# Kernel optimization log

Measured on AMD Instinct MI355X. Metric: run time of the kernel, lower is better.

## Reference

```python
import jax, jax.numpy as jnp
import numpy as np

DIM = 64
H = 4
POS_DIM = 4
NUM_IDS = 16
B = 2048
N = 64


def setup_inputs() -> dict:
    key = jax.random.key(0)
    ks = jax.random.split(key, 16)
    d8 = DIM // 8
    stdv = 1.0 / np.sqrt(DIM * DIM)
    inp = {
        "x": jax.random.normal(ks[0], (B, N, DIM), jnp.float32),
        "pos": jax.random.normal(ks[1], (B, N, POS_DIM), jnp.float32),
        "strength": jax.random.normal(ks[2], (512,), jnp.float32),
        "embed_id1": 3,
        # weights stored [in, out] (torch Linear weight transposed)
        "Wq": jax.random.normal(ks[3], (DIM, DIM), jnp.float32) * 0.05,
        "Wk": jax.random.normal(ks[4], (DIM, DIM), jnp.float32) * 0.05,
        "pos_W1": jax.random.normal(ks[5], (POS_DIM, POS_DIM), jnp.float32) * 0.3,
        "pos_b1": jnp.zeros((POS_DIM,), jnp.float32),
        "pos_W2": jax.random.normal(ks[6], (POS_DIM, d8), jnp.float32) * 0.3,
        "pos_b2": jnp.zeros((d8,), jnp.float32),
        "head_W": jax.random.normal(ks[7], (d8, H), jnp.float32) * 0.3,
        "head_b": jnp.zeros((H,), jnp.float32),
        "gate": jnp.ones((H,), jnp.float32),
        "embeds": jax.random.uniform(ks[8], (NUM_IDS, DIM * DIM), jnp.float32, -stdv, stdv),
        "out_W": jax.random.normal(ks[9], (DIM, DIM), jnp.float32) * 0.05,
        "out_b": jnp.zeros((DIM,), jnp.float32),
        "str_W": jax.random.normal(ks[10], (512, 64), jnp.float32) * 0.04,
        "str_b": jnp.zeros((64,), jnp.float32),
    }
    return inp


def reference(x, pos, strength, embed_id1, Wq, Wk, pos_W1, pos_b1, pos_W2, pos_b2,
              head_W, head_b, gate, embeds, out_W, out_b, str_W, str_b):
    Bb, Nn, dim = x.shape
    h = gate.shape[0]
    dh = dim // h

    # strength projection, added to dynamic-weight V
    s64 = strength @ str_W + str_b                       # [dim]
    E = embeds[embed_id1].reshape(dim, dim)              # per-sample V weight
    v = x @ E.T + s64                                    # F.linear(x, E) + strength
    v = v.reshape(Bb, Nn, h, dh).transpose(0, 2, 1, 3)   # [B,H,N,dh]

    # QK attention
    q = (x @ Wq).reshape(Bb, Nn, h, dh).transpose(0, 2, 1, 3)
    k = (x @ Wk).reshape(Bb, Nn, h, dh).transpose(0, 2, 1, 3)
    attn = jax.nn.softmax(jnp.einsum('bhqd,bhkd->bhqk', q, k) / np.sqrt(dh), axis=-1)

    # pairwise relative-position attention
    p = jax.nn.relu(pos @ pos_W1 + pos_b1) @ pos_W2 + pos_b2          # [B,N,dim//8]
    diff = p[:, :, None, :] - p[:, None, :, :]                        # [B,N,N,dim//8]
    pos_logits = jnp.einsum('bqkf,fh->bhqk', diff, head_W) + head_b[None, :, None, None]
    pos_attn = jax.nn.softmax(pos_logits, axis=-1)

    # sigmoid-gated mixing + renormalization
    g = jax.nn.sigmoid(gate)[None, :, None, None]
    attn = (1.0 - g) * attn + g * pos_attn
    attn = attn / jnp.sum(attn, axis=-1, keepdims=True)

    out = jnp.einsum('bhqk,bhkd->bhqd', attn, v)
    out = out.transpose(0, 2, 1, 3).reshape(Bb, Nn, dim)
    return out @ out_W + out_b
```

## Files before the change

### kernel.cpp

```cpp
#include <hip/hip_runtime.h>

typedef unsigned short u16;
typedef unsigned int u32;
typedef short bf8 __attribute__((ext_vector_type(8)));
typedef float f4v __attribute__((ext_vector_type(4)));
typedef float f16v __attribute__((ext_vector_type(16)));

#define STR 72

__device__ __forceinline__ u32 f2bf(float f){
    union{float f;u32 i;}c; c.f=f; u32 i=c.i;
    return (i + 0x7FFFu + ((i>>16)&1u)) >> 16;
}

__device__ __forceinline__ void stage_row16(const float* __restrict__ g, short* __restrict__ dst,
                                            int n, int c0){
    const float4* p = (const float4*)(g + n*64 + c0);
    float4 a=p[0], b=p[1], c=p[2], d=p[3];
    uint4 o0, o1;
    o0.x = f2bf(a.x)|(f2bf(a.y)<<16); o0.y = f2bf(a.z)|(f2bf(a.w)<<16);
    o0.z = f2bf(b.x)|(f2bf(b.y)<<16); o0.w = f2bf(b.z)|(f2bf(b.w)<<16);
    o1.x = f2bf(c.x)|(f2bf(c.y)<<16); o1.y = f2bf(c.z)|(f2bf(c.w)<<16);
    o1.z = f2bf(d.x)|(f2bf(d.y)<<16); o1.w = f2bf(d.z)|(f2bf(d.w)<<16);
    *(uint4*)&dst[n*STR + c0]     = o0;
    *(uint4*)&dst[n*STR + c0 + 8] = o1;
}

__device__ __forceinline__ void copy8k(const u16* __restrict__ src, short* __restrict__ dst, int t){
    const int r = t >> 2, cs = (t & 3) << 4;
    const uint4* s = (const uint4*)(src + r*64 + cs);
    uint4 a = s[0], b = s[1];
    *(uint4*)&dst[r*STR + cs]     = a;
    *(uint4*)&dst[r*STR + cs + 8] = b;
}

__device__ __forceinline__ void mmlin(const short* __restrict__ X, const short* __restrict__ Wt,
                                      int w, int l15, int quad, f4v c[4]){
    bf8 a0 = *(const bf8*)&X[(16*w + l15)*STR + quad*8];
    bf8 a1 = *(const bf8*)&X[(16*w + l15)*STR + 32 + quad*8];
    #pragma unroll
    for (int nt=0; nt<4; ++nt){
        bf8 b0 = *(const bf8*)&Wt[(16*nt + l15)*STR + quad*8];
        bf8 b1 = *(const bf8*)&Wt[(16*nt + l15)*STR + 32 + quad*8];
        c[nt] = __builtin_amdgcn_mfma_f32_16x16x32_bf16(a0, b0, c[nt], 0,0,0);
        c[nt] = __builtin_amdgcn_mfma_f32_16x16x32_bf16(a1, b1, c[nt], 0,0,0);
    }
}

__global__ __launch_bounds__(256) void pre_kernel(
    const float* __restrict__ pos, const float* __restrict__ strength,
    const int* __restrict__ embed_id,
    const float* __restrict__ Wq, const float* __restrict__ Wk,
    const float* __restrict__ pW1, const float* __restrict__ pb1,
    const float* __restrict__ pW2, const float* __restrict__ pb2,
    const float* __restrict__ hW, const float* __restrict__ embeds,
    const float* __restrict__ oW, const float* __restrict__ sW,
    const float* __restrict__ sb,
    float* __restrict__ ws_s64, float* __restrict__ ws_pat,
    u16* __restrict__ ws_wq, u16* __restrict__ ws_wk,
    u16* __restrict__ ws_ow, u16* __restrict__ ws_e, int B)
{
    const int blk = blockIdx.x;
    const int t = threadIdx.x;

    if (blk < B) {
        __shared__ float t_l[4][64];
        if (t < 64) {
            float pv[4], h1[4], p8[8];
            const float* gp = pos + ((size_t)blk*64 + t)*4;
            #pragma unroll
            for (int i = 0; i < 4; ++i) pv[i] = gp[i];
            #pragma unroll
            for (int j = 0; j < 4; ++j){
                float a = pb1[j];
                #pragma unroll
                for (int i = 0; i < 4; ++i) a = fmaf(pv[i], pW1[i*4+j], a);
                h1[j] = fmaxf(a, 0.f);
            }
            #pragma unroll
            for (int f = 0; f < 8; ++f){
                float a = pb2[f];
                #pragma unroll
                for (int j = 0; j < 4; ++j) a = fmaf(h1[j], pW2[j*8+f], a);
                p8[f] = a;
            }
            #pragma unroll
            for (int h = 0; h < 4; ++h){
                float a = 0.f;
                #pragma unroll
                for (int f = 0; f < 8; ++f) a = fmaf(p8[f], hW[f*4+h], a);
                t_l[h][t] = a;
            }
        }
        __syncthreads();
        const int h = t >> 6, k = t & 63;
        float v0 = -t_l[h][k];
        float m = v0;
        #pragma unroll
        for (int off = 32; off; off >>= 1) m = fmaxf(m, __shfl_xor(m, off));
        float e = __expf(v0 - m);
        float ssum = e;
        #pragma unroll
        for (int off = 32; off; off >>= 1) ssum += __shfl_xor(ssum, off);
        ws_pat[((size_t)blk*4 + h)*64 + k] = e / ssum;
        return;
    }

    const int j = blk - B;
    if (j < 3) {
        const float* W = (j==0) ? Wq : (j==1) ? Wk : oW;
        u16* dst = (j==0) ? ws_wq : (j==1) ? ws_wk : ws_ow;
        const int kp = t >> 3, ng = t & 7;
        const float4* r0 = (const float4*)(W + (2*kp  )*64 + 8*ng);
        const float4* r1 = (const float4*)(W + (2*kp+1)*64 + 8*ng);
        float4 a0=r0[0], a1=r0[1], b0=r1[0], b1=r1[1];
        float lo[8]={a0.x,a0.y,a0.z,a0.w,a1.x,a1.y,a1.z,a1.w};
        float hi[8]={b0.x,b0.y,b0.z,b0.w,b1.x,b1.y,b1.z,b1.w};
        #pragma unroll
        for (int i=0;i<8;++i)
            *(u32*)&dst[(8*ng+i)*64 + 2*kp] = f2bf(lo[i]) | (f2bf(hi[i])<<16);
    } else {
        __shared__ float sp[4][64];
        {
            const int n = t >> 2, c0 = (t & 3) << 4;
            const float4* p = (const float4*)(embeds + (size_t)(*embed_id)*4096 + n*64 + c0);
            float4 a=p[0], b=p[1], c=p[2], d=p[3];
            uint4 o0, o1;
            o0.x = f2bf(a.x)|(f2bf(a.y)<<16); o0.y = f2bf(a.z)|(f2bf(a.w)<<16);
            o0.z = f2bf(b.x)|(f2bf(b.y)<<16); o0.w = f2bf(b.z)|(f2bf(b.w)<<16);
            o1.x = f2bf(c.x)|(f2bf(c.y)<<16); o1.y = f2bf(c.z)|(f2bf(c.w)<<16);
            o1.z = f2bf(d.x)|(f2bf(d.y)<<16); o1.w = f2bf(d.z)|(f2bf(d.w)<<16);
            *(uint4*)&ws_e[n*64 + c0]     = o0;
            *(uint4*)&ws_e[n*64 + c0 + 8] = o1;
        }
        {
            const int d = t & 63, part = t >> 6;
            const float* wp = sW + part*128*64 + d;
            const float* s  = strength + part*128;
            float acc = 0.f;
            #pragma unroll 8
            for (int i = 0; i < 128; ++i) acc = fmaf(s[i], wp[i*64], acc);
            sp[part][d] = acc;
        }
        __syncthreads();
        if (t < 64) ws_s64[t] = sp[0][t] + sp[1][t] + sp[2][t] + sp[3][t] + sb[t];
    }
}

__global__ __launch_bounds__(256, 2) void attn_main_kernel(
    const float* __restrict__ x, const float* __restrict__ gate, const float* __restrict__ ob,
    const float* __restrict__ ws_s64, const float* __restrict__ ws_pat,
    const u16* __restrict__ ws_wq, const u16* __restrict__ ws_wk,
    const u16* __restrict__ ws_ow, const u16* __restrict__ ws_e,
    float* __restrict__ out)
{
    __shared__ short B0[64*STR];
    __shared__ short B1[64*STR];
    __shared__ short B2[64*STR];
    __shared__ short B3[64*STR];
    __shared__ short VT[64*STR];
    __shared__ short PX[64*STR];

    const int t    = threadIdx.x;
    const int b    = blockIdx.x;
    const int lane = t & 63;
    const int w    = t >> 6;
    const int l15  = lane & 15;
    const int l31  = lane & 31;
    const int l5   = lane >> 5;
    const int quad = lane >> 4;
    const int n    = t >> 2;
    const int c0   = (t & 3) << 4;

    stage_row16(x + (size_t)b*4096, B0, n, c0);
    copy8k(ws_wq, B1, t);
    copy8k(ws_wk, VT, t);

    uint4 eA, eB, owA, owB;
    {
        const int r = t >> 2, cs = (t & 3) << 4;
        const uint4* se = (const uint4*)(ws_e + r*64 + cs);
        eA = se[0]; eB = se[1];
        const uint4* so = (const uint4*)(ws_ow + r*64 + cs);
        owA = so[0]; owB = so[1];
    }
    float svv[4];
    #pragma unroll
    for (int nt=0;nt<4;++nt) svv[nt] = ws_s64[16*nt + l15];
    float g = 1.f/(1.f + __expf(-gate[w]));
    float obv[4];
    #pragma unroll
    for (int nt=0;nt<4;++nt) obv[nt] = ob[16*nt + l15];
    __syncthreads();

    {
        f4v cq[4], ck[4];
        #pragma unroll
        for (int nt=0;nt<4;++nt){
            cq[nt][0]=0.f;cq[nt][1]=0.f;cq[nt][2]=0.f;cq[nt][3]=0.f;
            ck[nt][0]=0.f;ck[nt][1]=0.f;ck[nt][2]=0.f;ck[nt][3]=0.f;
        }
        mmlin(B0, B1, w, l15, quad, cq);
        mmlin(B0, VT, w, l15, quad, ck);
        __syncthreads();
        #pragma unroll
        for (int nt=0;nt<4;++nt)
            #pragma unroll
            for (int r=0;r<4;++r){
                B2[(16*w + quad*4 + r)*STR + 16*nt + l15] = (short)f2bf(0.25f*cq[nt][r]);
                B3[(16*w + quad*4 + r)*STR + 16*nt + l15] = (short)f2bf(ck[nt][r]);
            }
        const int r = t >> 2, cs = (t & 3) << 4;
        *(uint4*)&B1[r*STR + cs]     = eA;
        *(uint4*)&B1[r*STR + cs + 8] = eB;
    }
    __syncthreads();

    {
        f4v c[4];
        #pragma unroll
        for (int nt=0;nt<4;++nt){ c[nt][0]=0.f;c[nt][1]=0.f;c[nt][2]=0.f;c[nt][3]=0.f; }
        mmlin(B0, B1, w, l15, quad, c);
        __syncthreads();
        #pragma unroll
        for (int nt=0;nt<4;++nt){
            float sv = svv[nt];
            uint2 pk;
            pk.x = f2bf(c[nt][0]+sv) | (f2bf(c[nt][1]+sv)<<16);
            pk.y = f2bf(c[nt][2]+sv) | (f2bf(c[nt][3]+sv)<<16);
            *(uint2*)&VT[(16*nt + l15)*STR + 16*w + quad*4] = pk;
        }
        const int r = t >> 2, cs = (t & 3) << 4;
        *(uint4*)&B1[r*STR + cs]     = owA;
        *(uint4*)&B1[r*STR + cs + 8] = owB;
    }
    __syncthreads();

    f16v S[2][2];
    {
        bf8 ka0 = *(const bf8*)&B3[(     l31)*STR + 16*w + 8*l5];
        bf8 ka1 = *(const bf8*)&B3[(32 + l31)*STR + 16*w + 8*l5];
        bf8 qb0 = *(const bf8*)&B2[(     l31)*STR + 16*w + 8*l5];
        bf8 qb1 = *(const bf8*)&B2[(32 + l31)*STR + 16*w + 8*l5];
        #pragma unroll
        for (int mt=0;mt<2;++mt)
            #pragma unroll
            for (int nt=0;nt<2;++nt)
                #pragma unroll
                for (int i=0;i<16;++i) S[mt][nt][i] = 0.f;
        S[0][0] = __builtin_amdgcn_mfma_f32_32x32x16_bf16(ka0, qb0, S[0][0], 0,0,0);
        S[0][1] = __builtin_amdgcn_mfma_f32_32x32x16_bf16(ka0, qb1, S[0][1], 0,0,0);
        S[1][0] = __builtin_amdgcn_mfma_f32_32x32x16_bf16(ka1, qb0, S[1][0], 0,0,0);
        S[1][1] = __builtin_amdgcn_mfma_f32_32x32x16_bf16(ka1, qb1, S[1][1], 0,0,0);
    }
    float ep[32];
    {
        const float* pp = ws_pat + ((size_t)b*4 + w)*64;
        #pragma unroll
        for (int mt=0;mt<2;++mt)
            #pragma unroll
            for (int rg=0;rg<4;++rg){
                float4 tv = *(const float4*)&pp[32*mt + 8*rg + 4*l5];
                ep[mt*16+rg*4+0] = g*tv.x; ep[mt*16+rg*4+1] = g*tv.y;
                ep[mt*16+rg*4+2] = g*tv.z; ep[mt*16+rg*4+3] = g*tv.w;
            }
    }
    float inv[2];
    #pragma unroll
    for (int nt=0;nt<2;++nt){
        float m = S[0][nt][0];
        #pragma unroll
        for (int i=1;i<16;++i) m = fmaxf(m, S[0][nt][i]);
        #pragma unroll
        for (int i=0;i<16;++i) m = fmaxf(m, S[1][nt][i]);
        m = fmaxf(m, __shfl_xor(m, 32));
        float l = 0.f;
        #pragma unroll
        for (int mt=0;mt<2;++mt)
            #pragma unroll
            for (int i=0;i<16;++i){ float e = __expf(S[mt][nt][i]-m); S[mt][nt][i] = e; l += e; }
        l += __shfl_xor(l, 32);
        float c1 = (1.f - g) / l;
        float tot = 0.f;
        #pragma unroll
        for (int mt=0;mt<2;++mt)
            #pragma unroll
            for (int i=0;i<16;++i){ float a = fmaf(c1, S[mt][nt][i], ep[mt*16+i]); S[mt][nt][i] = a; tot += a; }
        tot += __shfl_xor(tot, 32);
        inv[nt] = 1.f / tot;
    }
    __syncthreads();

    short* Pb = (w==0) ? B0 : (w==1) ? PX : (w==2) ? B2 : B3;
    #pragma unroll
    for (int nt=0;nt<2;++nt)
        #pragma unroll
        for (int mt=0;mt<2;++mt)
            #pragma unroll
            for (int rg=0;rg<4;++rg){
                float v0 = S[mt][nt][rg*4+0]*inv[nt], v1 = S[mt][nt][rg*4+1]*inv[nt];
                float v2 = S[mt][nt][rg*4+2]*inv[nt], v3 = S[mt][nt][rg*4+3]*inv[nt];
                uint2 pk;
                pk.x = f2bf(v0) | (f2bf(v1)<<16);
                pk.y = f2bf(v2) | (f2bf(v3)<<16);
                *(uint2*)&Pb[(32*nt + l31)*STR + 32*mt + 8*rg + 4*l5] = pk;
            }

    f4v o[4];
    {
        bf8 bv0 = *(const bf8*)&VT[(16*w + l15)*STR + quad*8];
        bf8 bv1 = *(const bf8*)&VT[(16*w + l15)*STR + 32 + quad*8];
        #pragma unroll
        for (int mt=0;mt<4;++mt){
            o[mt][0]=0.f;o[mt][1]=0.f;o[mt][2]=0.f;o[mt][3]=0.f;
            bf8 a0 = *(const bf8*)&Pb[(16*mt + l15)*STR + quad*8];
            bf8 a1 = *(const bf8*)&Pb[(16*mt + l15)*STR + 32 + quad*8];
            o[mt] = __builtin_amdgcn_mfma_f32_16x16x32_bf16(a0, bv0, o[mt], 0,0,0);
            o[mt] = __builtin_amdgcn_mfma_f32_16x16x32_bf16(a1, bv1, o[mt], 0,0,0);
        }
    }
    __syncthreads();

    #pragma unroll
    for (int mt=0;mt<4;++mt)
        #pragma unroll
        for (int r=0;r<4;++r)
            B3[(16*mt + quad*4 + r)*STR + 16*w + l15] = (short)f2bf(o[mt][r]);
    __syncthreads();

    {
        f4v c[4];
        #pragma unroll
        for (int nt=0;nt<4;++nt){
            c[nt][0]=obv[nt];c[nt][1]=obv[nt];c[nt][2]=obv[nt];c[nt][3]=obv[nt];
        }
        mmlin(B3, B1, w, l15, quad, c);
        #pragma unroll
        for (int nt=0;nt<4;++nt)
            #pragma unroll
            for (int r=0;r<4;++r)
                out[((size_t)b*64 + 16*w + quad*4 + r)*64 + 16*nt + l15] = c[nt][r];
    }
}

extern "C" void kernel_launch(void* const* d_in, const int* in_sizes, int n_in,
                              void* d_out, int out_size, void* d_ws, size_t ws_size,
                              hipStream_t stream) {
    const int B = in_sizes[0] / (64 * 64);

    float* ws_s64 = (float*)d_ws;
    float* ws_pat = ws_s64 + 64;
    u16*   ws_wq  = (u16*)(ws_pat + (size_t)B*4*64);
    u16*   ws_wk  = ws_wq + 4096;
    u16*   ws_ow  = ws_wk + 4096;
    u16*   ws_e   = ws_ow + 4096;

    pre_kernel<<<B + 4, 256, 0, stream>>>(
        (const float*)d_in[1],  (const float*)d_in[2],  (const int*)d_in[3],
        (const float*)d_in[4],  (const float*)d_in[5],
        (const float*)d_in[6],  (const float*)d_in[7],  (const float*)d_in[8],  (const float*)d_in[9],
        (const float*)d_in[10], (const float*)d_in[13], (const float*)d_in[14],
        (const float*)d_in[16], (const float*)d_in[17],
        ws_s64, ws_pat, ws_wq, ws_wk, ws_ow, ws_e, B);

    attn_main_kernel<<<B, 256, 0, stream>>>(
        (const float*)d_in[0],  (const float*)d_in[12], (const float*)d_in[15],
        ws_s64, ws_pat, ws_wq, ws_wk, ws_ow, ws_e,
        (float*)d_out);
}
```

Measured before the change: 140.4 us.

## Swizzle LDS layout, load x fragments directly to registers, drop barriers

Replaces the padded stride-72 shared-memory tiles with an XOR-swizzled 64-wide layout and cuts the LDS buffers from six to five. Each lane now loads and converts its own x MFMA operand fragments straight from global memory instead of staging x through LDS. The pos-attention prefetch moves before the first barrier, V is written into the freed K-weight buffer, and two synchronisations are removed. This is meant to lower LDS footprint (raising occupancy), bank conflicts and barrier count, at the cost of less coalesced global reads of x and more intricate index arithmetic.

```diff
diff --git a/kernel.cpp b/kernel.cpp
--- a/kernel.cpp
+++ b/kernel.cpp
@@ -6,45 +6,13 @@
 typedef float f4v __attribute__((ext_vector_type(4)));
 typedef float f16v __attribute__((ext_vector_type(16)));
 
-#define STR 72
-
 __device__ __forceinline__ u32 f2bf(float f){
     union{float f;u32 i;}c; c.f=f; u32 i=c.i;
     return (i + 0x7FFFu + ((i>>16)&1u)) >> 16;
 }
 
-__device__ __forceinline__ void stage_row16(const float* __restrict__ g, short* __restrict__ dst,
-                                            int n, int c0){
-    const float4* p = (const float4*)(g + n*64 + c0);
-    float4 a=p[0], b=p[1], c=p[2], d=p[3];
-    uint4 o0, o1;
-    o0.x = f2bf(a.x)|(f2bf(a.y)<<16); o0.y = f2bf(a.z)|(f2bf(a.w)<<16);
-    o0.z = f2bf(b.x)|(f2bf(b.y)<<16); o0.w = f2bf(b.z)|(f2bf(b.w)<<16);
-    o1.x = f2bf(c.x)|(f2bf(c.y)<<16); o1.y = f2bf(c.z)|(f2bf(c.w)<<16);
-    o1.z = f2bf(d.x)|(f2bf(d.y)<<16); o1.w = f2bf(d.z)|(f2bf(d.w)<<16);
-    *(uint4*)&dst[n*STR + c0]     = o0;
-    *(uint4*)&dst[n*STR + c0 + 8] = o1;
-}
-
-__device__ __forceinline__ void copy8k(const u16* __restrict__ src, short* __restrict__ dst, int t){
-    const int r = t >> 2, cs = (t & 3) << 4;
-    const uint4* s = (const uint4*)(src + r*64 + cs);
-    uint4 a = s[0], b = s[1];
-    *(uint4*)&dst[r*STR + cs]     = a;
-    *(uint4*)&dst[r*STR + cs + 8] = b;
-}
-
-__device__ __forceinline__ void mmlin(const short* __restrict__ X, const short* __restrict__ Wt,
-                                      int w, int l15, int quad, f4v c[4]){
-    bf8 a0 = *(const bf8*)&X[(16*w + l15)*STR + quad*8];
-    bf8 a1 = *(const bf8*)&X[(16*w + l15)*STR + 32 + quad*8];
-    #pragma unroll
-    for (int nt=0; nt<4; ++nt){
-        bf8 b0 = *(const bf8*)&Wt[(16*nt + l15)*STR + quad*8];
-        bf8 b1 = *(const bf8*)&Wt[(16*nt + l15)*STR + 32 + quad*8];
-        c[nt] = __builtin_amdgcn_mfma_f32_16x16x32_bf16(a0, b0, c[nt], 0,0,0);
-        c[nt] = __builtin_amdgcn_mfma_f32_16x16x32_bf16(a1, b1, c[nt], 0,0,0);
-    }
+__device__ __forceinline__ int sw(int row, int chunk){
+    return row*64 + ((chunk ^ (row & 7)) << 3);
 }
 
 __global__ __launch_bounds__(256) void pre_kernel(
@@ -154,12 +122,11 @@
     const u16* __restrict__ ws_ow, const u16* __restrict__ ws_e,
     float* __restrict__ out)
 {
-    __shared__ short B0[64*STR];
-    __shared__ short B1[64*STR];
-    __shared__ short B2[64*STR];
-    __shared__ short B3[64*STR];
-    __shared__ short VT[64*STR];
-    __shared__ short PX[64*STR];
+    __shared__ short W1[4096];
+    __shared__ short W2[4096];
+    __shared__ short QB[4096];
+    __shared__ short KB[4096];
+    __shared__ short PB[4096];
 
     const int t    = threadIdx.x;
     const int b    = blockIdx.x;
@@ -169,13 +136,30 @@
     const int l31  = lane & 31;
     const int l5   = lane >> 5;
     const int quad = lane >> 4;
-    const int n    = t >> 2;
-    const int c0   = (t & 3) << 4;
-
-    stage_row16(x + (size_t)b*4096, B0, n, c0);
-    copy8k(ws_wq, B1, t);
-    copy8k(ws_wk, VT, t);
-
+
+    {
+        const int r = t >> 2, cp = (t & 3) * 2;
+        const uint4* sq = (const uint4*)(ws_wq + r*64 + cp*8);
+        uint4 qa = sq[0], qb = sq[1];
+        *(uint4*)&W1[sw(r, cp)]   = qa;
+        *(uint4*)&W1[sw(r, cp+1)] = qb;
+        const uint4* sk = (const uint4*)(ws_wk + r*64 + cp*8);
+        uint4 ka = sk[0], kb = sk[1];
+        *(uint4*)&W2[sw(r, cp)]   = ka;
+        *(uint4*)&W2[sw(r, cp+1)] = kb;
+    }
+    bf8 xa0, xa1;
+    {
+        const float* xp = x + (size_t)b*4096 + (16*w + l15)*64 + quad*8;
+        float4 f0 = *(const float4*)xp,      f1 = *(const float4*)(xp+4);
+        float4 f2 = *(const float4*)(xp+32), f3 = *(const float4*)(xp+36);
+        union { short s[8]; bf8 v; } A0, A1;
+        A0.s[0]=(short)f2bf(f0.x); A0.s[1]=(short)f2bf(f0.y); A0.s[2]=(short)f2bf(f0.z); A0.s[3]=(short)f2bf(f0.w);
+        A0.s[4]=(short)f2bf(f1.x); A0.s[5]=(short)f2bf(f1.y); A0.s[6]=(short)f2bf(f1.z); A0.s[7]=(short)f2bf(f1.w);
+        A1.s[0]=(short)f2bf(f2.x); A1.s[1]=(short)f2bf(f2.y); A1.s[2]=(short)f2bf(f2.z); A1.s[3]=(short)f2bf(f2.w);
+        A1.s[4]=(short)f2bf(f3.x); A1.s[5]=(short)f2bf(f3.y); A1.s[6]=(short)f2bf(f3.z); A1.s[7]=(short)f2bf(f3.w);
+        xa0 = A0.v; xa1 = A1.v;
+    }
     uint4 eA, eB, owA, owB;
     {
         const int r = t >> 2, cs = (t & 3) << 4;
@@ -191,57 +175,80 @@
     float obv[4];
     #pragma unroll
     for (int nt=0;nt<4;++nt) obv[nt] = ob[16*nt + l15];
-    __syncthreads();
-
-    {
-        f4v cq[4], ck[4];
+    float ep[32];
+    {
+        const float* pp = ws_pat + ((size_t)b*4 + w)*64;
+        #pragma unroll
+        for (int mt=0;mt<2;++mt)
+            #pragma unroll
+            for (int rg=0;rg<4;++rg){
+                float4 tv = *(const float4*)&pp[32*mt + 8*rg + 4*l5];
+                ep[mt*16+rg*4+0] = g*tv.x; ep[mt*16+rg*4+1] = g*tv.y;
+                ep[mt*16+rg*4+2] = g*tv.z; ep[mt*16+rg*4+3] = g*tv.w;
+            }
+    }
+    __syncthreads();
+
+    f4v cq[4], ck[4];
+    #pragma unroll
+    for (int nt=0;nt<4;++nt){
+        cq[nt][0]=0.f;cq[nt][1]=0.f;cq[nt][2]=0.f;cq[nt][3]=0.f;
+        ck[nt][0]=0.f;ck[nt][1]=0.f;ck[nt][2]=0.f;ck[nt][3]=0.f;
+        bf8 b0 = *(const bf8*)&W1[sw(16*nt+l15, quad)];
+        bf8 b1 = *(const bf8*)&W1[sw(16*nt+l15, quad+4)];
+        cq[nt] = __builtin_amdgcn_mfma_f32_16x16x32_bf16(xa0, b0, cq[nt], 0,0,0);
+        cq[nt] = __builtin_amdgcn_mfma_f32_16x16x32_bf16(xa1, b1, cq[nt], 0,0,0);
+        bf8 d0 = *(const bf8*)&W2[sw(16*nt+l15, quad)];
+        bf8 d1 = *(const bf8*)&W2[sw(16*nt+l15, quad+4)];
+        ck[nt] = __builtin_amdgcn_mfma_f32_16x16x32_bf16(xa0, d0, ck[nt], 0,0,0);
+        ck[nt] = __builtin_amdgcn_mfma_f32_16x16x32_bf16(xa1, d1, ck[nt], 0,0,0);
+    }
+    __syncthreads();
+
+    #pragma unroll
+    for (int nt=0;nt<4;++nt){
+        const int ch = 2*nt + (l15>>3), off = l15 & 7;
+        #pragma unroll
+        for (int r=0;r<4;++r){
+            const int row = 16*w + quad*4 + r;
+            QB[sw(row, ch) + off] = (short)f2bf(0.25f*cq[nt][r]);
+            KB[sw(row, ch) + off] = (short)f2bf(ck[nt][r]);
+        }
+    }
+    {
+        const int r = t >> 2, cp = (t & 3) * 2;
+        *(uint4*)&W1[sw(r, cp)]   = eA;
+        *(uint4*)&W1[sw(r, cp+1)] = eB;
+    }
+    __syncthreads();
+
+    {
+        f4v cv[4];
         #pragma unroll
         for (int nt=0;nt<4;++nt){
-            cq[nt][0]=0.f;cq[nt][1]=0.f;cq[nt][2]=0.f;cq[nt][3]=0.f;
-            ck[nt][0]=0.f;ck[nt][1]=0.f;ck[nt][2]=0.f;ck[nt][3]=0.f;
-        }
-        mmlin(B0, B1, w, l15, quad, cq);
-        mmlin(B0, VT, w, l15, quad, ck);
-        __syncthreads();
-        #pragma unroll
-        for (int nt=0;nt<4;++nt)
-            #pragma unroll
-            for (int r=0;r<4;++r){
-                B2[(16*w + quad*4 + r)*STR + 16*nt + l15] = (short)f2bf(0.25f*cq[nt][r]);
-                B3[(16*w + quad*4 + r)*STR + 16*nt + l15] = (short)f2bf(ck[nt][r]);
-            }
-        const int r = t >> 2, cs = (t & 3) << 4;
-        *(uint4*)&B1[r*STR + cs]     = eA;
-        *(uint4*)&B1[r*STR + cs + 8] = eB;
-    }
-    __syncthreads();
-
-    {
-        f4v c[4];
-        #pragma unroll
-        for (int nt=0;nt<4;++nt){ c[nt][0]=0.f;c[nt][1]=0.f;c[nt][2]=0.f;c[nt][3]=0.f; }
-        mmlin(B0, B1, w, l15, quad, c);
-        __syncthreads();
+            cv[nt][0]=0.f;cv[nt][1]=0.f;cv[nt][2]=0.f;cv[nt][3]=0.f;
+            bf8 b0 = *(const bf8*)&W1[sw(16*nt+l15, quad)];
+            bf8 b1 = *(const bf8*)&W1[sw(16*nt+l15, quad+4)];
+            cv[nt] = __builtin_amdgcn_mfma_f32_16x16x32_bf16(xa0, b0, cv[nt], 0,0,0);
+            cv[nt] = __builtin_amdgcn_mfma_f32_16x16x32_bf16(xa1, b1, cv[nt], 0,0,0);
+        }
+        const int ch = 2*w + (quad>>1), off = (quad&1)*4;
         #pragma unroll
         for (int nt=0;nt<4;++nt){
             float sv = svv[nt];
             uint2 pk;
-            pk.x = f2bf(c[nt][0]+sv) | (f2bf(c[nt][1]+sv)<<16);
-            pk.y = f2bf(c[nt][2]+sv) | (f2bf(c[nt][3]+sv)<<16);
-            *(uint2*)&VT[(16*nt + l15)*STR + 16*w + quad*4] = pk;
-        }
-        const int r = t >> 2, cs = (t & 3) << 4;
-        *(uint4*)&B1[r*STR + cs]     = owA;
-        *(uint4*)&B1[r*STR + cs + 8] = owB;
-    }
-    __syncthreads();
+            pk.x = f2bf(cv[nt][0]+sv) | (f2bf(cv[nt][1]+sv)<<16);
+            pk.y = f2bf(cv[nt][2]+sv) | (f2bf(cv[nt][3]+sv)<<16);
+            *(uint2*)&W2[sw(16*nt+l15, ch) + off] = pk;
+        }
+    }
 
     f16v S[2][2];
     {
-        bf8 ka0 = *(const bf8*)&B3[(     l31)*STR + 16*w + 8*l5];
-        bf8 ka1 = *(const bf8*)&B3[(32 + l31)*STR + 16*w + 8*l5];
-        bf8 qb0 = *(const bf8*)&B2[(     l31)*STR + 16*w + 8*l5];
-        bf8 qb1 = *(const bf8*)&B2[(32 + l31)*STR + 16*w + 8*l5];
+        bf8 ka0 = *(const bf8*)&KB[sw(     l31, 2*w + l5)];
+        bf8 ka1 = *(const bf8*)&KB[sw(32 + l31, 2*w + l5)];
+        bf8 qb0 = *(const bf8*)&QB[sw(     l31, 2*w + l5)];
+        bf8 qb1 = *(const bf8*)&QB[sw(32 + l31, 2*w + l5)];
         #pragma unroll
         for (int mt=0;mt<2;++mt)
             #pragma unroll
@@ -253,18 +260,6 @@
         S[1][0] = __builtin_amdgcn_mfma_f32_32x32x16_bf16(ka1, qb0, S[1][0], 0,0,0);
         S[1][1] = __builtin_amdgcn_mfma_f32_32x32x16_bf16(ka1, qb1, S[1][1], 0,0,0);
     }
-    float ep[32];
-    {
-        const float* pp = ws_pat + ((size_t)b*4 + w)*64;
-        #pragma unroll
-        for (int mt=0;mt<2;++mt)
-            #pragma unroll
-            for (int rg=0;rg<4;++rg){
-                float4 tv = *(const float4*)&pp[32*mt + 8*rg + 4*l5];
-                ep[mt*16+rg*4+0] = g*tv.x; ep[mt*16+rg*4+1] = g*tv.y;
-                ep[mt*16+rg*4+2] = g*tv.z; ep[mt*16+rg*4+3] = g*tv.w;
-            }
-    }
     float inv[2];
     #pragma unroll
     for (int nt=0;nt<2;++nt){
@@ -291,7 +286,7 @@
     }
     __syncthreads();
 
-    short* Pb = (w==0) ? B0 : (w==1) ? PX : (w==2) ? B2 : B3;
+    short* Pb = (w==0) ? W1 : (w==1) ? PB : (w==2) ? QB : KB;
     #pragma unroll
     for (int nt=0;nt<2;++nt)
         #pragma unroll
@@ -303,43 +298,52 @@
                 uint2 pk;
                 pk.x = f2bf(v0) | (f2bf(v1)<<16);
                 pk.y = f2bf(v2) | (f2bf(v3)<<16);
-                *(uint2*)&Pb[(32*nt + l31)*STR + 32*mt + 8*rg + 4*l5] = pk;
+                *(uint2*)&Pb[sw(32*nt + l31, 4*mt + rg) + 4*l5] = pk;
             }
 
     f4v o[4];
     {
-        bf8 bv0 = *(const bf8*)&VT[(16*w + l15)*STR + quad*8];
-        bf8 bv1 = *(const bf8*)&VT[(16*w + l15)*STR + 32 + quad*8];
+        bf8 bv0 = *(const bf8*)&W2[sw(16*w+l15, quad)];
+        bf8 bv1 = *(const bf8*)&W2[sw(16*w+l15, quad+4)];
         #pragma unroll
         for (int mt=0;mt<4;++mt){
             o[mt][0]=0.f;o[mt][1]=0.f;o[mt][2]=0.f;o[mt][3]=0.f;
-            bf8 a0 = *(const bf8*)&Pb[(16*mt + l15)*STR + quad*8];
-            bf8 a1 = *(const bf8*)&Pb[(16*mt + l15)*STR + 32 + quad*8];
+            bf8 a0 = *(const bf8*)&Pb[sw(16*mt+l15, quad)];
+            bf8 a1 = *(const bf8*)&Pb[sw(16*mt+l15, quad+4)];
             o[mt] = __builtin_amdgcn_mfma_f32_16x16x32_bf16(a0, bv0, o[mt], 0,0,0);
             o[mt] = __builtin_amdgcn_mfma_f32_16x16x32_bf16(a1, bv1, o[mt], 0,0,0);
         }
     }
     __syncthreads();
 
-    #pragma unroll
-    for (int mt=0;mt<4;++mt)
-        #pragma unroll
-        for (int r=0;r<4;++r)
-            B3[(16*mt + quad*4 + r)*STR + 16*w + l15] = (short)f2bf(o[mt][r]);
-    __syncthreads();
-
-    {
-        f4v c[4];
+    {
+        const int ch = 2*w + (l15>>3), off = l15 & 7;
+        #pragma unroll
+        for (int mt=0;mt<4;++mt)
+            #pragma unroll
+            for (int r=0;r<4;++r)
+                QB[sw(16*mt + quad*4 + r, ch) + off] = (short)f2bf(o[mt][r]);
+        const int rr = t >> 2, cp = (t & 3) * 2;
+        *(uint4*)&W1[sw(rr, cp)]   = owA;
+        *(uint4*)&W1[sw(rr, cp+1)] = owB;
+    }
+    __syncthreads();
+
+    {
+        bf8 a0 = *(const bf8*)&QB[sw(16*w+l15, quad)];
+        bf8 a1 = *(const bf8*)&QB[sw(16*w+l15, quad+4)];
         #pragma unroll
         for (int nt=0;nt<4;++nt){
-            c[nt][0]=obv[nt];c[nt][1]=obv[nt];c[nt][2]=obv[nt];c[nt][3]=obv[nt];
-        }
-        mmlin(B3, B1, w, l15, quad, c);
-        #pragma unroll
-        for (int nt=0;nt<4;++nt)
+            f4v c;
+            c[0]=obv[nt];c[1]=obv[nt];c[2]=obv[nt];c[3]=obv[nt];
+            bf8 b0 = *(const bf8*)&W1[sw(16*nt+l15, quad)];
+            bf8 b1 = *(const bf8*)&W1[sw(16*nt+l15, quad+4)];
+            c = __builtin_amdgcn_mfma_f32_16x16x32_bf16(a0, b0, c, 0,0,0);
+            c = __builtin_amdgcn_mfma_f32_16x16x32_bf16(a1, b1, c, 0,0,0);
             #pragma unroll
             for (int r=0;r<4;++r)
-                out[((size_t)b*64 + 16*w + quad*4 + r)*64 + 16*nt + l15] = c[nt][r];
+                out[((size_t)b*64 + 16*w + quad*4 + r)*64 + 16*nt + l15] = c[r];
+        }
     }
 }
 
```

Result: no change. 141.5 us (+0.8%).
